# Optimization experiments

Hardware: AMD Instinct MI355X
Metric: run time of the kernel (lower is better)

The kernel has to match this reference:

```python
import jax, jax.numpy as jnp
import numpy as np


def setup_inputs() -> dict:
    key = jax.random.key(0)
    k1, k2, k3, k4 = jax.random.split(key, 4)
    B, S, IN, H = 4, 2048, 512, 1024
    x = jax.random.normal(k1, (B, S, IN), dtype=jnp.float32)
    W1 = jax.random.normal(k2, (IN, H), dtype=jnp.float32) * (1.0 / np.sqrt(IN))
    b1 = jax.random.normal(k3, (H,), dtype=jnp.float32) * 0.02
    Wq = jax.random.normal(k4, (H, H), dtype=jnp.float32) * (1.0 / np.sqrt(H))
    return {"x": x, "W1": W1, "b1": b1, "Wq": Wq, "atten_size": 16}


def reference(x, W1, b1, Wq, atten_size):
    A = atten_size
    B, S, _ = x.shape
    H = W1.shape[1]
    h = jax.nn.relu(jnp.einsum('bsi,ih->bsh', x, W1) + b1)  # [B,S,H]
    # zero-pad sequence dim by A on each side
    padded = jnp.pad(h, ((0, 0), (A, A), (0, 0)))  # [B,S+2A,H]
    # torch: stack(roll(padded, k, 1) for k in -A..A, dim=2) then slice [A:-A]
    # => x_nei[b, i, j] = padded[b, 2A + i - j]
    idx = 2 * A + jnp.arange(S)[:, None] - jnp.arange(2 * A + 1)[None, :]  # [S,W]
    x_nei = padded[:, idx, :]  # [B,S,W,H]
    q = jnp.einsum('bsh,hk->bsk', h, Wq)  # [B,S,H]
    scores = jnp.einsum('bsh,bswh->bsw', q, x_nei) / jnp.sqrt(jnp.asarray(H, x.dtype))
    w = jax.nn.softmax(scores, axis=2)  # softmax over window axis
    out = jnp.einsum('bsw,bswh->bsh', w, x_nei)
    return out
```

## Files before the change

### kernel.cpp

```cpp
#include <hip/hip_runtime.h>
#include <stdint.h>

constexpr int BATCH = 4;
constexpr int SEQ   = 2048;
constexpr int DIN   = 512;
constexpr int DH    = 1024;
constexpr int BS    = BATCH * SEQ;
constexpr int AP    = 32;
constexpr int AW    = 64;

typedef float  floatx4 __attribute__((ext_vector_type(4)));
typedef short  bf16x8  __attribute__((ext_vector_type(8)));

static __device__ __forceinline__ unsigned short f2bf(float f) {
  union { float f; unsigned u; } v; v.f = f;
  unsigned r = (v.u + 0x7fffu + ((v.u >> 16) & 1u)) >> 16;
  return (unsigned short)r;
}

static __device__ __forceinline__ void gld_lds16(const unsigned short* g, const short* l) {
  typedef const __attribute__((address_space(1))) void* gvp;
  typedef __attribute__((address_space(3))) void* lvp;
  __builtin_amdgcn_global_load_lds((gvp)(uintptr_t)g, (lvp)(unsigned)(uintptr_t)l, 16, 0, 0);
}

__global__ __launch_bounds__(256) void to_bf16_k(const float* __restrict__ in,
                                                 unsigned short* __restrict__ out, int n) {
  int i = (blockIdx.x * 256 + threadIdx.x) * 4;
  if (i < n) {
    float4 v = *(const float4*)(in + i);
    ushort4 o;
    o.x = f2bf(v.x); o.y = f2bf(v.y); o.z = f2bf(v.z); o.w = f2bf(v.w);
    *(ushort4*)(out + i) = o;
  }
}

__global__ __launch_bounds__(256) void transpose_bf16_k(const float* __restrict__ in,
                                                        unsigned short* __restrict__ out,
                                                        int R, int C) {
  __shared__ float t[32][33];
  int c0 = blockIdx.x * 32, r0 = blockIdx.y * 32;
  int tx = threadIdx.x & 31, ty = threadIdx.x >> 5;
  for (int i = ty; i < 32; i += 8) t[i][tx] = in[(size_t)(r0 + i) * C + c0 + tx];
  __syncthreads();
  for (int i = ty; i < 32; i += 8) out[(size_t)(c0 + i) * R + r0 + tx] = f2bf(t[tx][i]);
}

__global__ __launch_bounds__(256) void transpose_hb_k(const unsigned short* __restrict__ in,
                                                      unsigned short* __restrict__ out) {
  __shared__ __align__(16) unsigned short t[64][80];
  const int tid = threadIdx.x;
  const int r0 = blockIdx.x * 64;
  const int c0 = blockIdx.y * 64;
  const int tr = tid >> 2, tc = (tid & 3) * 16;
  const uint4* src = (const uint4*)(in + (size_t)(r0 + tr) * DH + c0 + tc);
  uint4 v0 = src[0], v1 = src[1];
  *(uint4*)&t[tr][tc]     = v0;
  *(uint4*)&t[tr][tc + 8] = v1;
  __syncthreads();
  __align__(16) unsigned short vals[16];
  #pragma unroll
  for (int e = 0; e < 16; e++) vals[e] = t[tc + e][tr];
  uint4* dst = (uint4*)(out + (size_t)(c0 + tr) * BS + r0 + tc);
  dst[0] = ((uint4*)vals)[0];
  dst[1] = ((uint4*)vals)[1];
}

template <bool RELU>
__global__ __launch_bounds__(256) void gemm_bt(const unsigned short* __restrict__ Ab,
                                               const unsigned short* __restrict__ Bt,
                                               const float* __restrict__ bias,
                                               unsigned short* __restrict__ outB,
                                               int M, int N, int K) {
  __shared__ __align__(16) short As[128 * 32];
  __shared__ __align__(16) short Bs[128 * 32];
  const int tid  = threadIdx.x;
  const int m0   = blockIdx.y * 128, n0 = blockIdx.x * 128;
  const int wv   = tid >> 6, lane = tid & 63;
  const int wm   = (wv >> 1) * 64, wn = (wv & 1) * 64;
  const int l16  = lane & 15, quad = lane >> 4;

  const int ra = lane >> 2;
  const int ca = (lane & 3) * 8;
  const unsigned short* gA0 = Ab + (size_t)(m0 + wv * 32 + ra) * K + ca;
  const unsigned short* gA1 = Ab + (size_t)(m0 + wv * 32 + 16 + ra) * K + ca;
  const unsigned short* gB0 = Bt + (size_t)(n0 + wv * 32 + ra) * K + ca;
  const unsigned short* gB1 = Bt + (size_t)(n0 + wv * 32 + 16 + ra) * K + ca;
  const short* lA0 = &As[wv * 1024];
  const short* lA1 = &As[wv * 1024 + 512];
  const short* lB0 = &Bs[wv * 1024];
  const short* lB1 = &Bs[wv * 1024 + 512];

  floatx4 acc[4][4];
  for (int i = 0; i < 4; i++)
    for (int j = 0; j < 4; j++) acc[i][j] = {0.f, 0.f, 0.f, 0.f};

  const int ksteps = K >> 5;
  for (int ks = 0; ks < ksteps; ++ks) {
    __syncthreads();
    gld_lds16(gA0, lA0); gld_lds16(gA1, lA1);
    gld_lds16(gB0, lB0); gld_lds16(gB1, lB1);
    gA0 += 32; gA1 += 32; gB0 += 32; gB1 += 32;
    __syncthreads();
    bf16x8 af[4], bfr[4];
    for (int i = 0; i < 4; i++)
      af[i] = *(const bf16x8*)&As[(wm + i * 16 + l16) * 32 + quad * 8];
    for (int j = 0; j < 4; j++)
      bfr[j] = *(const bf16x8*)&Bs[(wn + j * 16 + l16) * 32 + quad * 8];
    for (int i = 0; i < 4; i++)
      for (int j = 0; j < 4; j++)
        acc[i][j] = __builtin_amdgcn_mfma_f32_16x16x32_bf16(af[i], bfr[j], acc[i][j], 0, 0, 0);
  }

  for (int j = 0; j < 4; j++) {
    const int col = n0 + wn + j * 16 + l16;
    const float bv = RELU ? bias[col] : 0.f;
    for (int i = 0; i < 4; i++) {
      const int rowb = m0 + wm + i * 16 + quad * 4;
      for (int r = 0; r < 4; r++) {
        float v = acc[i][j][r] + bv;
        if (RELU) v = fmaxf(v, 0.f);
        outB[(size_t)(rowb + r) * N + col] = f2bf(v);
      }
    }
  }
}

__global__ __launch_bounds__(512) void attn_mfma_k(const unsigned short* __restrict__ hb,
                                                   const unsigned short* __restrict__ hbT,
                                                   const unsigned short* __restrict__ qb,
                                                   float* __restrict__ out) {
  __shared__ float Sf[32 * 64];
  __shared__ __align__(16) short Ps[32 * 72];

  const int tid  = threadIdx.x;
  const int wave = tid >> 6, lane = tid & 63;
  const int l16  = lane & 15, quad = lane >> 4;
  const int p0   = blockIdx.x * AP;
  const int s0   = p0 & (SEQ - 1);

  for (int i = tid; i < 32 * 72 / 2; i += 512) ((unsigned*)Ps)[i] = 0;

  {
    const int mt = wave >> 2, nt = wave & 3;
    const unsigned short* qp = qb + (size_t)(p0 + mt * 16 + l16) * DH + quad * 8;
    const int hrow = s0 - 16 + nt * 16 + l16;
    const bool hv = (hrow >= 0) && (hrow < SEQ);
    const unsigned short* hp = hb + (long long)(p0 - 16 + nt * 16 + l16) * DH + quad * 8;

    floatx4 ac[4] = {{0,0,0,0},{0,0,0,0},{0,0,0,0},{0,0,0,0}};
    const bf16x8 hz = {0,0,0,0,0,0,0,0};
    #pragma unroll
    for (int it = 0; it < 32; ++it) {
      bf16x8 qa = *(const bf16x8*)(qp + it * 32);
      bf16x8 ha = hz;
      if (hv) ha = *(const bf16x8*)(hp + it * 32);
      ac[it & 3] = __builtin_amdgcn_mfma_f32_16x16x32_bf16(qa, ha, ac[it & 3], 0, 0, 0);
    }
    floatx4 s4;
    for (int r = 0; r < 4; r++)
      s4[r] = (ac[0][r] + ac[1][r]) + (ac[2][r] + ac[3][r]);
    for (int r = 0; r < 4; r++)
      Sf[(mt * 16 + quad * 4 + r) * 64 + nt * 16 + l16] = s4[r] * (1.f / 32.f);
  }
  __syncthreads();

  {
    const int row = tid >> 4, k = tid & 15;
    const float v0 = Sf[row * 64 + row + k];
    const float v1 = Sf[row * 64 + row + k + 16];
    const float v2 = (k == 0) ? Sf[row * 64 + row + 32] : -1e30f;
    float mx = fmaxf(v0, fmaxf(v1, v2));
    for (int off = 1; off < 16; off <<= 1) mx = fmaxf(mx, __shfl_xor(mx, off, 64));
    const float e0 = __expf(v0 - mx), e1 = __expf(v1 - mx);
    const float e2 = (k == 0) ? __expf(v2 - mx) : 0.f;
    float sum = e0 + e1 + e2;
    for (int off = 1; off < 16; off <<= 1) sum += __shfl_xor(sum, off, 64);
    const float inv = 1.f / sum;
    Ps[row * 72 + row + k] = f2bf(e0 * inv);
    Ps[row * 72 + row + k + 16] = f2bf(e1 * inv);
    if (k == 0) Ps[row * 72 + row + 32] = f2bf(e2 * inv);
  }
  __syncthreads();

  {
    const int nt2 = wave >> 2;
    const bf16x8 pb0 = *(const bf16x8*)&Ps[(nt2 * 16 + l16) * 72 + quad * 8];
    const bf16x8 pb1 = *(const bf16x8*)&Ps[(nt2 * 16 + l16) * 72 + 32 + quad * 8];

    int lo = 16 - s0; if (lo < 0) lo = 0;
    int hi = SEQ + 16 - s0; if (hi > AW) hi = AW;
    const bool interior = (lo == 0) && (hi == AW);

    #pragma unroll
    for (int i = 0; i < 16; ++i) {
      const int mt2 = (wave & 3) * 16 + i;
      const unsigned short* ap = hbT + (size_t)(mt2 * 16 + l16) * BS + (p0 - 16) + quad * 8;
      bf16x8 aa0 = *(const bf16x8*)(ap);
      bf16x8 aa1 = *(const bf16x8*)(ap + 32);
      if (!interior) {
        #pragma unroll
        for (int j = 0; j < 8; j++) {
          const int k = quad * 8 + j;
          if (k < lo || k >= hi) aa0[j] = 0;
          if (k + 32 < lo || k + 32 >= hi) aa1[j] = 0;
        }
      }
      floatx4 o = {0.f, 0.f, 0.f, 0.f};
      o = __builtin_amdgcn_mfma_f32_16x16x32_bf16(aa0, pb0, o, 0, 0, 0);
      o = __builtin_amdgcn_mfma_f32_16x16x32_bf16(aa1, pb1, o, 0, 0, 0);
      float4 st; st.x = o[0]; st.y = o[1]; st.z = o[2]; st.w = o[3];
      *(float4*)(out + (size_t)(p0 + nt2 * 16 + l16) * DH + mt2 * 16 + quad * 4) = st;
    }
  }
}

extern "C" void kernel_launch(void* const* d_in, const int* in_sizes, int n_in,
                              void* d_out, int out_size, void* d_ws, size_t ws_size,
                              hipStream_t stream) {
  const float* x  = (const float*)d_in[0];
  const float* W1 = (const float*)d_in[1];
  const float* b1 = (const float*)d_in[2];
  const float* Wq = (const float*)d_in[3];

  char* w = (char*)d_ws;
  unsigned short* xb  = (unsigned short*)(w);
  unsigned short* w1t = (unsigned short*)(w + (8ull  << 20));
  unsigned short* wqt = (unsigned short*)(w + (9ull  << 20));
  unsigned short* hb  = (unsigned short*)(w + (11ull << 20));
  unsigned short* hbT = (unsigned short*)(w + (27ull << 20));
  unsigned short* qb  = (unsigned short*)(w + (43ull << 20));

  to_bf16_k<<<(BS * DIN) / (256 * 4), 256, 0, stream>>>(x, xb, BS * DIN);
  transpose_bf16_k<<<dim3(DH / 32, DIN / 32), 256, 0, stream>>>(W1, w1t, DIN, DH);
  transpose_bf16_k<<<dim3(DH / 32, DH / 32), 256, 0, stream>>>(Wq, wqt, DH, DH);

  gemm_bt<true><<<dim3(DH / 128, BS / 128), 256, 0, stream>>>(xb, w1t, b1, hb, BS, DH, DIN);
  transpose_hb_k<<<dim3(BS / 64, DH / 64), 256, 0, stream>>>(hb, hbT);
  gemm_bt<false><<<dim3(DH / 128, BS / 128), 256, 0, stream>>>(hb, wqt, nullptr, qb, BS, DH, DH);

  attn_mfma_k<<<BS / AP, 512, 0, stream>>>(hb, hbT, qb, (float*)d_out);
}
```

Measured before the change: 174.3 us.

## Fuse x fp32-to-bf16 conversion and h transpose into first GEMM

The first GEMM now loads fp32 x directly, converts it to bf16 in registers and writes it into LDS, which removes the separate conversion kernel and its round trip through global memory. Its epilogue also writes the transposed copy of h, which removes the standalone transpose kernel. The grid is reordered so blockIdx.x walks M. In exchange, the A operand loses the async global-to-LDS path, and the transposed stores are narrow 8-byte writes with a large stride.

```diff
diff --git a/kernel.cpp b/kernel.cpp
--- a/kernel.cpp
+++ b/kernel.cpp
@@ -22,17 +22,6 @@
   typedef const __attribute__((address_space(1))) void* gvp;
   typedef __attribute__((address_space(3))) void* lvp;
   __builtin_amdgcn_global_load_lds((gvp)(uintptr_t)g, (lvp)(unsigned)(uintptr_t)l, 16, 0, 0);
-}
-
-__global__ __launch_bounds__(256) void to_bf16_k(const float* __restrict__ in,
-                                                 unsigned short* __restrict__ out, int n) {
-  int i = (blockIdx.x * 256 + threadIdx.x) * 4;
-  if (i < n) {
-    float4 v = *(const float4*)(in + i);
-    ushort4 o;
-    o.x = f2bf(v.x); o.y = f2bf(v.y); o.z = f2bf(v.z); o.w = f2bf(v.w);
-    *(ushort4*)(out + i) = o;
-  }
 }
 
 __global__ __launch_bounds__(256) void transpose_bf16_k(const float* __restrict__ in,
@@ -46,42 +35,85 @@
   for (int i = ty; i < 32; i += 8) out[(size_t)(c0 + i) * R + r0 + tx] = f2bf(t[tx][i]);
 }
 
-__global__ __launch_bounds__(256) void transpose_hb_k(const unsigned short* __restrict__ in,
-                                                      unsigned short* __restrict__ out) {
-  __shared__ __align__(16) unsigned short t[64][80];
-  const int tid = threadIdx.x;
-  const int r0 = blockIdx.x * 64;
-  const int c0 = blockIdx.y * 64;
-  const int tr = tid >> 2, tc = (tid & 3) * 16;
-  const uint4* src = (const uint4*)(in + (size_t)(r0 + tr) * DH + c0 + tc);
-  uint4 v0 = src[0], v1 = src[1];
-  *(uint4*)&t[tr][tc]     = v0;
-  *(uint4*)&t[tr][tc + 8] = v1;
-  __syncthreads();
-  __align__(16) unsigned short vals[16];
-  #pragma unroll
-  for (int e = 0; e < 16; e++) vals[e] = t[tc + e][tr];
-  uint4* dst = (uint4*)(out + (size_t)(c0 + tr) * BS + r0 + tc);
-  dst[0] = ((uint4*)vals)[0];
-  dst[1] = ((uint4*)vals)[1];
-}
-
-template <bool RELU>
-__global__ __launch_bounds__(256) void gemm_bt(const unsigned short* __restrict__ Ab,
+__global__ __launch_bounds__(256) void gemm1_k(const float* __restrict__ X,
                                                const unsigned short* __restrict__ Bt,
                                                const float* __restrict__ bias,
                                                unsigned short* __restrict__ outB,
-                                               int M, int N, int K) {
+                                               unsigned short* __restrict__ outBT) {
+  const int M = BS, N = DH, K = DIN;
   __shared__ __align__(16) short As[128 * 32];
   __shared__ __align__(16) short Bs[128 * 32];
   const int tid  = threadIdx.x;
-  const int m0   = blockIdx.y * 128, n0 = blockIdx.x * 128;
+  const int m0   = blockIdx.x * 128, n0 = blockIdx.y * 128;
   const int wv   = tid >> 6, lane = tid & 63;
   const int wm   = (wv >> 1) * 64, wn = (wv & 1) * 64;
   const int l16  = lane & 15, quad = lane >> 4;
 
-  const int ra = lane >> 2;
-  const int ca = (lane & 3) * 8;
+  const int ar = tid >> 1, acol = (tid & 1) * 16;
+  const float* gX = X + (size_t)(m0 + ar) * K + acol;
+  short* lA = &As[ar * 32 + acol];
+  const int ra = lane >> 2, ca = (lane & 3) * 8;
+  const unsigned short* gB0 = Bt + (size_t)(n0 + wv * 32 + ra) * K + ca;
+  const unsigned short* gB1 = Bt + (size_t)(n0 + wv * 32 + 16 + ra) * K + ca;
+  const short* lB0 = &Bs[wv * 1024];
+  const short* lB1 = &Bs[wv * 1024 + 512];
+
+  floatx4 acc[4][4];
+  for (int i = 0; i < 4; i++)
+    for (int j = 0; j < 4; j++) acc[i][j] = {0.f, 0.f, 0.f, 0.f};
+
+  for (int ks = 0; ks < K / 32; ++ks) {
+    float4 x0 = ((const float4*)gX)[0], x1 = ((const float4*)gX)[1];
+    float4 x2 = ((const float4*)gX)[2], x3 = ((const float4*)gX)[3];
+    gX += 32;
+    __syncthreads();
+    gld_lds16(gB0, lB0); gld_lds16(gB1, lB1);
+    gB0 += 32; gB1 += 32;
+    __align__(16) unsigned short cv[16];
+    cv[0] = f2bf(x0.x); cv[1] = f2bf(x0.y); cv[2]  = f2bf(x0.z); cv[3]  = f2bf(x0.w);
+    cv[4] = f2bf(x1.x); cv[5] = f2bf(x1.y); cv[6]  = f2bf(x1.z); cv[7]  = f2bf(x1.w);
+    cv[8] = f2bf(x2.x); cv[9] = f2bf(x2.y); cv[10] = f2bf(x2.z); cv[11] = f2bf(x2.w);
+    cv[12] = f2bf(x3.x); cv[13] = f2bf(x3.y); cv[14] = f2bf(x3.z); cv[15] = f2bf(x3.w);
+    ((uint4*)lA)[0] = ((uint4*)cv)[0];
+    ((uint4*)lA)[1] = ((uint4*)cv)[1];
+    __syncthreads();
+    bf16x8 af[4], bfr[4];
+    for (int i = 0; i < 4; i++)
+      af[i] = *(const bf16x8*)&As[(wm + i * 16 + l16) * 32 + quad * 8];
+    for (int j = 0; j < 4; j++)
+      bfr[j] = *(const bf16x8*)&Bs[(wn + j * 16 + l16) * 32 + quad * 8];
+    for (int i = 0; i < 4; i++)
+      for (int j = 0; j < 4; j++)
+        acc[i][j] = __builtin_amdgcn_mfma_f32_16x16x32_bf16(af[i], bfr[j], acc[i][j], 0, 0, 0);
+  }
+
+  for (int j = 0; j < 4; j++) {
+    const int col = n0 + wn + j * 16 + l16;
+    const float bv = bias[col];
+    for (int i = 0; i < 4; i++) {
+      const int rowb = m0 + wm + i * 16 + quad * 4;
+      float v[4];
+      for (int r = 0; r < 4; r++) v[r] = fmaxf(acc[i][j][r] + bv, 0.f);
+      for (int r = 0; r < 4; r++) outB[(size_t)(rowb + r) * N + col] = f2bf(v[r]);
+      ushort4 o4; o4.x = f2bf(v[0]); o4.y = f2bf(v[1]); o4.z = f2bf(v[2]); o4.w = f2bf(v[3]);
+      *(ushort4*)(outBT + (size_t)col * M + rowb) = o4;
+    }
+  }
+}
+
+__global__ __launch_bounds__(256) void gemm2_k(const unsigned short* __restrict__ Ab,
+                                               const unsigned short* __restrict__ Bt,
+                                               unsigned short* __restrict__ outB) {
+  const int N = DH, K = DH;
+  __shared__ __align__(16) short As[128 * 32];
+  __shared__ __align__(16) short Bs[128 * 32];
+  const int tid  = threadIdx.x;
+  const int m0   = blockIdx.x * 128, n0 = blockIdx.y * 128;
+  const int wv   = tid >> 6, lane = tid & 63;
+  const int wm   = (wv >> 1) * 64, wn = (wv & 1) * 64;
+  const int l16  = lane & 15, quad = lane >> 4;
+
+  const int ra = lane >> 2, ca = (lane & 3) * 8;
   const unsigned short* gA0 = Ab + (size_t)(m0 + wv * 32 + ra) * K + ca;
   const unsigned short* gA1 = Ab + (size_t)(m0 + wv * 32 + 16 + ra) * K + ca;
   const unsigned short* gB0 = Bt + (size_t)(n0 + wv * 32 + ra) * K + ca;
@@ -95,8 +127,7 @@
   for (int i = 0; i < 4; i++)
     for (int j = 0; j < 4; j++) acc[i][j] = {0.f, 0.f, 0.f, 0.f};
 
-  const int ksteps = K >> 5;
-  for (int ks = 0; ks < ksteps; ++ks) {
+  for (int ks = 0; ks < K / 32; ++ks) {
     __syncthreads();
     gld_lds16(gA0, lA0); gld_lds16(gA1, lA1);
     gld_lds16(gB0, lB0); gld_lds16(gB1, lB1);
@@ -114,14 +145,10 @@
 
   for (int j = 0; j < 4; j++) {
     const int col = n0 + wn + j * 16 + l16;
-    const float bv = RELU ? bias[col] : 0.f;
     for (int i = 0; i < 4; i++) {
       const int rowb = m0 + wm + i * 16 + quad * 4;
-      for (int r = 0; r < 4; r++) {
-        float v = acc[i][j][r] + bv;
-        if (RELU) v = fmaxf(v, 0.f);
-        outB[(size_t)(rowb + r) * N + col] = f2bf(v);
-      }
+      for (int r = 0; r < 4; r++)
+        outB[(size_t)(rowb + r) * N + col] = f2bf(acc[i][j][r]);
     }
   }
 }
@@ -224,20 +251,17 @@
   const float* Wq = (const float*)d_in[3];
 
   char* w = (char*)d_ws;
-  unsigned short* xb  = (unsigned short*)(w);
-  unsigned short* w1t = (unsigned short*)(w + (8ull  << 20));
-  unsigned short* wqt = (unsigned short*)(w + (9ull  << 20));
-  unsigned short* hb  = (unsigned short*)(w + (11ull << 20));
-  unsigned short* hbT = (unsigned short*)(w + (27ull << 20));
-  unsigned short* qb  = (unsigned short*)(w + (43ull << 20));
-
-  to_bf16_k<<<(BS * DIN) / (256 * 4), 256, 0, stream>>>(x, xb, BS * DIN);
+  unsigned short* w1t = (unsigned short*)(w);
+  unsigned short* wqt = (unsigned short*)(w + (1ull  << 20));
+  unsigned short* hb  = (unsigned short*)(w + (3ull  << 20));
+  unsigned short* hbT = (unsigned short*)(w + (19ull << 20));
+  unsigned short* qb  = (unsigned short*)(w + (35ull << 20));
+
   transpose_bf16_k<<<dim3(DH / 32, DIN / 32), 256, 0, stream>>>(W1, w1t, DIN, DH);
   transpose_bf16_k<<<dim3(DH / 32, DH / 32), 256, 0, stream>>>(Wq, wqt, DH, DH);
 
-  gemm_bt<true><<<dim3(DH / 128, BS / 128), 256, 0, stream>>>(xb, w1t, b1, hb, BS, DH, DIN);
-  transpose_hb_k<<<dim3(BS / 64, DH / 64), 256, 0, stream>>>(hb, hbT);
-  gemm_bt<false><<<dim3(DH / 128, BS / 128), 256, 0, stream>>>(hb, wqt, nullptr, qb, BS, DH, DH);
+  gemm1_k<<<dim3(BS / 128, DH / 128), 256, 0, stream>>>(x, w1t, b1, hb, hbT);
+  gemm2_k<<<dim3(BS / 128, DH / 128), 256, 0, stream>>>(hb, wqt, qb);
 
   attn_mfma_k<<<BS / AP, 512, 0, stream>>>(hb, hbT, qb, (float*)d_out);
 }
```

Measured after the change: 162.7 us. -6.6%, faster.
